# Performance work log

Hardware: AMD Instinct MI355X
Metric: run time of the kernel (lower is better)

## Reference

```python
import jax, jax.numpy as jnp
import numpy as np

N = 384      # max_nodes
H = 256      # layers[0] == layers[1] == layers[2]
Z = 128      # dim_z
ED = 128     # edge_dim
AH = ED // 2 # attention hidden

# complete directed graph: combinations (i<j) then reversed pairs
_i, _j = np.triu_indices(N, k=1)
_SRC = jnp.asarray(np.concatenate([_i, _j]), dtype=jnp.int32)  # edge_index[0]
_DST = jnp.asarray(np.concatenate([_j, _i]), dtype=jnp.int32)  # edge_index[1]


def setup_inputs() -> dict:
    key = jax.random.key(0)
    ks = jax.random.split(key, 16)
    def p(k, shape, fan_in):
        return jax.random.normal(k, shape, dtype=jnp.float32) * (1.0 / np.sqrt(fan_in))
    return {
        "z": jax.random.normal(ks[0], (1, Z), dtype=jnp.float32),
        # GRU (torch layout: W_ih [3H, Z], W_hh [3H, H]; gate order r, z, n)
        "gru_Wih": p(ks[1], (3 * H, Z), Z),
        "gru_Whh": p(ks[2], (3 * H, H), H),
        "gru_bih": jnp.zeros((3 * H,), jnp.float32),
        "gru_bhh": jnp.zeros((3 * H,), jnp.float32),
        # edge_generator MLP: 2H -> 4H -> ED
        "eg_W1": p(ks[3], (2 * H, 4 * H), 2 * H), "eg_b1": jnp.zeros((4 * H,), jnp.float32),
        "eg_W2": p(ks[4], (4 * H, ED), 4 * H),   "eg_b2": jnp.zeros((ED,), jnp.float32),
        # attention MLPs: (ED+H) -> ED//2 -> 1
        "att0_W1": p(ks[5], (ED + H, AH), ED + H), "att0_b1": jnp.zeros((AH,), jnp.float32),
        "att0_W2": p(ks[6], (AH, 1), AH),           "att0_b2": jnp.zeros((1,), jnp.float32),
        "att1_W1": p(ks[7], (ED + H, AH), ED + H), "att1_b1": jnp.zeros((AH,), jnp.float32),
        "att1_W2": p(ks[8], (AH, 1), AH),           "att1_b2": jnp.zeros((1,), jnp.float32),
        # EdgeConv output linears: H -> H
        "conv0_W": p(ks[9], (H, H), H),  "conv0_b": jnp.zeros((H,), jnp.float32),
        "conv1_W": p(ks[10], (H, H), H), "conv1_b": jnp.zeros((H,), jnp.float32),
    }


def _forward(z, gru_Wih, gru_Whh, gru_bih, gru_bhh,
             eg_W1, eg_b1, eg_W2, eg_b2,
             att0_W1, att0_b1, att0_W2, att0_b2,
             att1_W1, att1_b1, att1_W2, att1_b2,
             conv0_W, conv0_b, conv1_W, conv1_b):
    # --- GRU node generation: input is the same latent z at every step ---
    gi = z[0] @ gru_Wih.T + gru_bih            # [3H], constant per step
    gir, giz, gin = jnp.split(gi, 3)
    def step(h, _):
        gh = h @ gru_Whh.T + gru_bhh
        ghr, ghz, ghn = jnp.split(gh, 3)
        r = jax.nn.sigmoid(gir + ghr)
        u = jax.nn.sigmoid(giz + ghz)
        n = jnp.tanh(gin + r * ghn)
        h2 = (1.0 - u) * n + u * h
        return h2, h2
    _, nodes = jax.lax.scan(step, jnp.zeros((H,), z.dtype), None, length=N)  # [N, H]

    # --- edge features over the complete directed graph ---
    pairs = jnp.concatenate([nodes[_SRC], nodes[_DST]], axis=-1)            # [E, 2H]
    edges = jax.nn.relu(pairs @ eg_W1 + eg_b1) @ eg_W2 + eg_b2              # [E, ED]

    # --- EdgeConv: gather src, attention MLP gate, scatter-sum, linear ---
    def conv(x, aW1, ab1, aW2, ab2, W, b):
        xs = x[_SRC]                                                        # [E, H]
        a_in = jnp.concatenate([edges, xs], axis=-1)                        # [E, ED+H]
        att = jax.nn.sigmoid(jax.nn.relu(a_in @ aW1 + ab1) @ aW2 + ab2)     # [E, 1]
        agg = jax.ops.segment_sum(att * xs, _DST, num_segments=N)           # [N, H]
        return agg @ W + b

    x = jax.nn.relu(conv(nodes, att0_W1, att0_b1, att0_W2, att0_b2, conv0_W, conv0_b))
    x = conv(x, att1_W1, att1_b1, att1_W2, att1_b2, conv1_W, conv1_b)
    return jnp.sum(x, axis=0)                                               # [H]


def reference(z, gru_Wih, gru_Whh, gru_bih, gru_bhh,
              eg_W1, eg_b1, eg_W2, eg_b2,
              att0_W1, att0_b1, att0_W2, att0_b2,
              att1_W1, att1_b1, att1_W2, att1_b2,
              conv0_W, conv0_b, conv1_W, conv1_b):
    return _forward(z, gru_Wih, gru_Whh, gru_bih, gru_bhh,
                    eg_W1, eg_b1, eg_W2, eg_b2,
                    att0_W1, att0_b1, att0_W2, att0_b2,
                    att1_W1, att1_b1, att1_W2, att1_b2,
                    conv0_W, conv0_b, conv1_W, conv1_b)
```

## Files before the change

### kernel.cpp

```cpp
#include <hip/hip_runtime.h>
#include <hip/hip_fp16.h>
#include <cstdint>

#define DEV static __device__ __forceinline__

typedef _Float16 h2v __attribute__((ext_vector_type(2)));
typedef _Float16 half8 __attribute__((ext_vector_type(8)));
typedef float float4v __attribute__((ext_vector_type(4)));

union U32H2 { uint32_t u; _Float16 f[2]; };

DEV uint32_t pack_f2(float a, float b) {
    auto p = __builtin_amdgcn_cvt_pkrtz(a, b);
    return __builtin_bit_cast(uint32_t, p);
}

DEV half8 bc8(uint4 v) { return __builtin_bit_cast(half8, v); }

DEV float sigmoidf_(float x) { return 1.0f / (1.0f + __expf(-x)); }

DEV void gl_lds16(const void* gsrc, void* ldst) {
    __builtin_amdgcn_global_load_lds(
        (const __attribute__((address_space(1))) uint32_t*)gsrc,
        (__attribute__((address_space(3))) uint32_t*)ldst, 16, 0, 0);
}

DEV float pick4(float4v lo, float4v hi, int bsel, int r) {
    float v0 = bsel ? hi[0] : lo[0];
    float v1 = bsel ? hi[1] : lo[1];
    float v2 = bsel ? hi[2] : lo[2];
    float v3 = bsel ? hi[3] : lo[3];
    float x01 = (r & 1) ? v1 : v0;
    float x23 = (r & 1) ? v3 : v2;
    return (r & 2) ? x23 : x01;
}

static const size_t OFF_W16T  = 0;
static const size_t OFF_GI    = 98304;
static const size_t OFF_CC    = 99072;
static const size_t OFF_BF    = 99200;
static const size_t OFF_NODES = 164736;
static const size_t OFF_PF    = 263040;
static const size_t OFF_QF    = 459648;
static const size_t OFF_R0    = 656256;
static const size_t OFF_R1    = 680832;
static const size_t OFF_TT    = 705408;
static const size_t OFF_ATT0  = 10142592;
static const size_t OFF_ATT1  = 10290048;
static const size_t OFF_AGG   = 10437504;
static const size_t OFF_X0    = 10535808;
static const size_t OFF_CS    = 10634112;
static const size_t OFF_V     = 10634496;
static const size_t WS_TOTAL  = 10634752;

__global__ void k_prep_all(const float* __restrict__ Whh, uint32_t* __restrict__ WL,
                           const float* __restrict__ z, const float* __restrict__ Wih,
                           const float* __restrict__ bih, const float* __restrict__ bhh,
                           float* __restrict__ gs,
                           const float* __restrict__ egb2, const float* __restrict__ a0W1,
                           const float* __restrict__ a1W1, float* __restrict__ cc,
                           const float* __restrict__ egW2, uint32_t* __restrict__ BF) {
    int bb = blockIdx.x;
    if (bb < 96) {
        int o4 = bb * 256 + threadIdx.x;
        int c = o4 >> 9, t = o4 & 511;
        int rt = c >> 3, kt = c & 7;
        int lane = t & 63, wv = t >> 6;
        int row = (rt >> 1) * 256 + wv * 32 + ((rt & 1) << 4) + (lane & 15);
        int k0 = kt*32 + (lane >> 4)*8;
        const float* src = Whh + row*256 + k0;
        uint4 o;
        o.x = pack_f2(src[0], src[1]);
        o.y = pack_f2(src[2], src[3]);
        o.z = pack_f2(src[4], src[5]);
        o.w = pack_f2(src[6], src[7]);
        ((uint4*)WL)[o4] = o;
    } else if (bb < 99) {
        int o = (bb - 96) * 256 + threadIdx.x;
        float acc = bih[o];
        if (o < 512) acc += bhh[o];
        for (int i = 0; i < 128; ++i) acc += Wih[o*128 + i] * z[i];
        gs[o] = acc;
    } else if (bb == 99) {
        int t = threadIdx.x;
        if (t < 128) {
            const float* A = (t < 64) ? a0W1 : a1W1;
            int j = t & 63;
            float acc = 0.f;
            for (int i = 0; i < 128; ++i) acc += egb2[i] * A[i*64 + j];
            cc[t] = acc;
        }
    } else {
        int idx = (bb - 100) * 256 + threadIdx.x;
        int k2 = idx >> 7, n = idx & 127;
        const float* A = (n < 64) ? (a0W1 + n) : (a1W1 + (n - 64));
        const float* w0 = egW2 + (2*k2) * 128;
        float a = 0.f, b = 0.f;
        for (int i = 0; i < 128; ++i) {
            float av = A[i*64];
            a += w0[i] * av;
            b += w0[128 + i] * av;
        }
        int kk = k2 >> 4, jgrp = (k2 >> 2) & 3, sub = k2 & 3;
        int lane = jgrp*16 + (n & 15), t = n >> 4;
        BF[((kk*8 + t)*64 + lane)*4 + sub] = pack_f2(a, b);
    }
}

__global__ void __launch_bounds__(512, 2)
k_gru(const float* __restrict__ gs, const float* __restrict__ bhh,
      const uint32_t* __restrict__ WL, float* __restrict__ nodes) {
    int tid = threadIdx.x;
    int lane = tid & 63, wv = tid >> 6;
    int kq = lane >> 4, c = lane & 15;
    __shared__ __align__(16) _Float16 hh16[512];

    uint4 w[48];
    const uint4* wl4 = (const uint4*)WL;
    #pragma unroll
    for (int cc = 0; cc < 48; ++cc) w[cc] = wl4[cc*512 + tid];
    #pragma unroll
    for (int cc = 0; cc < 48; ++cc)
        asm volatile("" : "+a"(w[cc].x), "+a"(w[cc].y), "+a"(w[cc].z), "+a"(w[cc].w));

    const float L2E = 1.44269504088896f;
    int r = c & 3, bsel = (c >> 2) & 1;
    int i_loc = kq*4 + r + bsel*16;
    int gidx = wv*32 + i_loc;
    float pr = -L2E * gs[gidx];
    float pz = -L2E * gs[256 + gidx];
    float gin_l = gs[512 + gidx];
    float bn_l  = bhh[512 + gidx];
    float pn = -2.f * L2E * gin_l;
    bool active = (c < 8);

    float h = 0.f;
    if (tid < 256) ((uint32_t*)hh16)[tid] = 0u;
    __syncthreads();

    const float4v z4 = {0.f, 0.f, 0.f, 0.f};
    int par = 0;
    for (int t = 0; t < 384; ++t) {
        const _Float16* hb = hh16 + par*256 + kq*8;
        uint4 b[8];
        #pragma unroll
        for (int kt = 0; kt < 8; ++kt) b[kt] = *(const uint4*)(hb + kt*32);

        float4v d0, d1, d2, d3, d4, d5;
        d0 = __builtin_amdgcn_mfma_f32_16x16x32_f16(bc8(w[0]),  bc8(b[0]), z4, 0, 0, 0);
        d1 = __builtin_amdgcn_mfma_f32_16x16x32_f16(bc8(w[8]),  bc8(b[0]), z4, 0, 0, 0);
        #pragma unroll
        for (int kt = 1; kt < 8; ++kt) {
            d0 = __builtin_amdgcn_mfma_f32_16x16x32_f16(bc8(w[kt]),    bc8(b[kt]), d0, 0, 0, 0);
            d1 = __builtin_amdgcn_mfma_f32_16x16x32_f16(bc8(w[8+kt]),  bc8(b[kt]), d1, 0, 0, 0);
        }
        float ghr = pick4(d0, d1, bsel, r);
        float er = __builtin_amdgcn_exp2f(__builtin_fmaf(ghr, -L2E, pr));
        float rg = __builtin_amdgcn_rcpf(1.f + er);

        d2 = __builtin_amdgcn_mfma_f32_16x16x32_f16(bc8(w[16]), bc8(b[0]), z4, 0, 0, 0);
        d3 = __builtin_amdgcn_mfma_f32_16x16x32_f16(bc8(w[24]), bc8(b[0]), z4, 0, 0, 0);
        d4 = __builtin_amdgcn_mfma_f32_16x16x32_f16(bc8(w[32]), bc8(b[0]), z4, 0, 0, 0);
        d5 = __builtin_amdgcn_mfma_f32_16x16x32_f16(bc8(w[40]), bc8(b[0]), z4, 0, 0, 0);
        #pragma unroll
        for (int kt = 1; kt < 8; ++kt) {
            d2 = __builtin_amdgcn_mfma_f32_16x16x32_f16(bc8(w[16+kt]), bc8(b[kt]), d2, 0, 0, 0);
            d3 = __builtin_amdgcn_mfma_f32_16x16x32_f16(bc8(w[24+kt]), bc8(b[kt]), d3, 0, 0, 0);
            d4 = __builtin_amdgcn_mfma_f32_16x16x32_f16(bc8(w[32+kt]), bc8(b[kt]), d4, 0, 0, 0);
            d5 = __builtin_amdgcn_mfma_f32_16x16x32_f16(bc8(w[40+kt]), bc8(b[kt]), d5, 0, 0, 0);
        }

        float ghz = pick4(d2, d3, bsel, r);
        float ghn = pick4(d4, d5, bsel, r);
        float eu = __builtin_amdgcn_exp2f(__builtin_fmaf(ghz, -L2E, pz));
        float u  = __builtin_amdgcn_rcpf(1.f + eu);
        float tm = ghn + bn_l;
        float q  = __builtin_fmaf(rg * tm, -2.f * L2E, pn);
        float e2 = __builtin_amdgcn_exp2f(q);
        float nn = __builtin_fmaf(2.f, __builtin_amdgcn_rcpf(1.f + e2), -1.f);
        h = nn + u * (h - nn);

        if (active) {
            hh16[(par ^ 1)*256 + gidx] = (_Float16)h;
            nodes[t*256 + gidx] = h;
        }
        asm volatile("s_waitcnt lgkmcnt(0)" ::: "memory");
        __builtin_amdgcn_sched_barrier(0);
        __builtin_amdgcn_s_barrier();
        __builtin_amdgcn_sched_barrier(0);
        par ^= 1;
    }
}

__global__ void k_pq(const float* __restrict__ nodes, const float* __restrict__ eg_W1,
                     const float* __restrict__ eg_b1, const float* __restrict__ a0W1,
                     const float* __restrict__ a0b1, const float* __restrict__ cc,
                     uint32_t* __restrict__ PF, uint32_t* __restrict__ QF,
                     float* __restrict__ R0) {
    int tid = threadIdx.x;
    int s0 = blockIdx.x * 4;
    __shared__ float ns[4][256];
    #pragma unroll
    for (int q = 0; q < 4; ++q) ns[q][tid] = nodes[(s0+q)*256 + tid];
    __syncthreads();

    int k0 = tid * 4;
    float acc[4][4];
    #pragma unroll
    for (int q = 0; q < 4; ++q) { acc[q][0]=0;acc[q][1]=0;acc[q][2]=0;acc[q][3]=0; }
    for (int i = 0; i < 256; ++i) {
        float4 wv = *(const float4*)&eg_W1[i*1024 + k0];
        #pragma unroll
        for (int q = 0; q < 4; ++q) {
            float nv = ns[q][i];
            acc[q][0] += nv*wv.x; acc[q][1] += nv*wv.y;
            acc[q][2] += nv*wv.z; acc[q][3] += nv*wv.w;
        }
    }
    float4 bv = *(const float4*)&eg_b1[k0];
    {
        int kk = k0 >> 5;
        int lgrp = ((k0 >> 3) & 3) * 16;
        int sub = (k0 & 7) >> 1;
        #pragma unroll
        for (int q = 0; q < 4; ++q) {
            int s = s0 + q, g = s >> 4, srow = s & 15;
            uint2 pw;
            pw.x = pack_f2(acc[q][0] + bv.x, acc[q][1] + bv.y);
            pw.y = pack_f2(acc[q][2] + bv.z, acc[q][3] + bv.w);
            *(uint2*)(PF + (((g*32 + kk)*64 + lgrp + srow) << 2) + sub) = pw;
        }
    }

    #pragma unroll
    for (int q = 0; q < 4; ++q) { acc[q][0]=0;acc[q][1]=0;acc[q][2]=0;acc[q][3]=0; }
    for (int i = 0; i < 256; ++i) {
        float4 wv = *(const float4*)&eg_W1[(256+i)*1024 + k0];
        #pragma unroll
        for (int q = 0; q < 4; ++q) {
            float nv = ns[q][i];
            acc[q][0] += nv*wv.x; acc[q][1] += nv*wv.y;
            acc[q][2] += nv*wv.z; acc[q][3] += nv*wv.w;
        }
    }
    #pragma unroll
    for (int q = 0; q < 4; ++q) {
        uint2 pw;
        pw.x = pack_f2(acc[q][0], acc[q][1]);
        pw.y = pack_f2(acc[q][2], acc[q][3]);
        ((uint2*)QF)[(s0+q)*256 + tid] = pw;
    }

    int srow = tid >> 6, j = tid & 63;
    float racc = a0b1[j] + cc[j];
    for (int i = 0; i < 256; ++i) racc += ns[srow][i] * a0W1[(128+i)*64 + j];
    R0[(s0+srow)*64 + j] = racc;
}

DEV void stageA(const uint32_t* __restrict__ PF, const uint32_t* __restrict__ BF,
                int g, int hc, char* buf, int tid) {
    const char* psrc = (const char*)(PF + ((size_t)g*32 + (size_t)hc*2) * 256);
    if (tid < 128) gl_lds16(psrc + tid*16, buf + tid*16);
    const char* bsrc = (const char*)(BF + (size_t)hc * 4096);
    #pragma unroll
    for (int i = 0; i < 4; ++i)
        gl_lds16(bsrc + tid*16 + i*4096, buf + 2048 + tid*16 + i*4096);
}

__global__ void __launch_bounds__(256, 2)
k_phaseA_mfma(const uint32_t* __restrict__ PF, const uint32_t* __restrict__ QF,
              const uint32_t* __restrict__ BF, uint32_t* __restrict__ TT) {
    __shared__ __align__(16) char smem[69632];
    uint4* Qs4 = (uint4*)smem;
    char* bufbase = smem + 32768;

    int tid = threadIdx.x;
    int lane = tid & 63, wv = tid >> 6;
    int g = blockIdx.x, d0 = blockIdx.y * 16;

    {
        const char* src = (const char*)(QF + (size_t)d0 * 512);
        int off = tid * 16;
        #pragma unroll
        for (int i = 0; i < 8; ++i)
            gl_lds16(src + off + i*4096, (char*)Qs4 + off + i*4096);
    }
    stageA(PF, BF, g, 0, bufbase, tid);
    asm volatile("s_waitcnt vmcnt(0)" ::: "memory");
    __builtin_amdgcn_sched_barrier(0);
    __builtin_amdgcn_s_barrier();
    __builtin_amdgcn_sched_barrier(0);

    float4v acc[4][8];
    #pragma unroll
    for (int t = 0; t < 4; ++t)
        #pragma unroll
        for (int n = 0; n < 8; ++n) acc[t][n] = 0.f;

    for (int hc = 0; hc < 16; ++hc) {
        char* cur = bufbase + (hc & 1) * 18432;
        char* nxt = bufbase + ((hc + 1) & 1) * 18432;
        if (hc < 15) stageA(PF, BF, g, hc + 1, nxt, tid);

        uint4* Ph = (uint4*)cur;
        uint4* Bh = (uint4*)(cur + 2048);
        #pragma unroll
        for (int kkl = 0; kkl < 2; ++kkl) {
            int kkg = hc*2 + kkl;
            half8 b[8];
            #pragma unroll
            for (int n = 0; n < 8; ++n) b[n] = bc8(Bh[(kkl*8 + n)*64 + lane]);
            half8 p8 = bc8(Ph[kkl*64 + lane]);
            #pragma unroll
            for (int t = 0; t < 4; ++t) {
                half8 q8 = bc8(Qs4[(wv*4 + t)*128 + kkg*4 + (lane >> 4)]);
                half8 x = p8 + q8;
                half8 zz = 0;
                x = __builtin_elementwise_max(x, zz);
                #pragma unroll
                for (int n = 0; n < 8; ++n)
                    acc[t][n] = __builtin_amdgcn_mfma_f32_16x16x32_f16(x, b[n], acc[t][n], 0, 0, 0);
            }
        }
        asm volatile("s_waitcnt vmcnt(0)" ::: "memory");
        __builtin_amdgcn_sched_barrier(0);
        __builtin_amdgcn_s_barrier();
        __builtin_amdgcn_sched_barrier(0);
    }

    _Float16* epi = (_Float16*)(smem + 32768);
    int cn = lane & 15, rhi = (lane >> 4) * 4;
    for (int half = 0; half < 2; ++half) {
        __syncthreads();
        #pragma unroll
        for (int t = 0; t < 4; ++t) {
            int dl = wv*4 + t;
            #pragma unroll
            for (int n = 0; n < 4; ++n) {
                int j = n*16 + cn;
                float4v v = acc[t][half*4 + n];
                #pragma unroll
                for (int r = 0; r < 4; ++r)
                    epi[((rhi + r)*16 + dl)*64 + j] = (_Float16)v[r];
            }
        }
        __syncthreads();
        int srow = tid >> 4, dl = tid & 15;
        const uint4* src = (const uint4*)(epi + tid*64);
        uint4* dst = (uint4*)(TT + ((size_t)((g*16 + srow)*384 + d0 + dl))*64 + half*32);
        #pragma unroll
        for (int q = 0; q < 8; ++q) dst[q] = src[q];
    }
}

__global__ void k_att(const uint32_t* __restrict__ TT, const float* __restrict__ R,
                      const float* __restrict__ w2, const float* __restrict__ b2,
                      int off, float* __restrict__ ATT, float* __restrict__ CS) {
    int tid = threadIdx.x;
    int p = blockIdx.x * 256 + tid;
    int s = p / 384, d = p - s * 384;
    int sa = (blockIdx.x * 256) / 384;
    __shared__ float w2s[64];
    __shared__ float rs[2][64];
    if (tid < 64) w2s[tid] = w2[tid];
    else if (tid < 128) rs[0][tid - 64] = R[sa*64 + (tid - 64)];
    else if (tid < 192) {
        int sb = sa + 1;
        rs[1][tid - 128] = (sb < 384) ? R[sb*64 + (tid - 128)] : 0.f;
    }
    __syncthreads();
    const uint4* tp = (const uint4*)(TT + (size_t)p*64 + off);
    const float* rp = (s == sa) ? rs[0] : rs[1];
    float logit = b2[0];
    #pragma unroll
    for (int m = 0; m < 8; ++m) {
        uint4 tv = tp[m];
        uint32_t us[4] = {tv.x, tv.y, tv.z, tv.w};
        #pragma unroll
        for (int q = 0; q < 4; ++q) {
            U32H2 c; c.u = us[q];
            int j = m*8 + q*2;
            float h0 = fmaxf((float)c.f[0] + rp[j],   0.f);
            float h1 = fmaxf((float)c.f[1] + rp[j+1], 0.f);
            logit += h0*w2s[j] + h1*w2s[j+1];
        }
    }
    float a = 1.f / (1.f + __expf(-logit));
    float a_eff = (s == d) ? 0.f : a;
    ATT[p] = a_eff;

    if (CS) {
        float va = (s == sa) ? a_eff : 0.f;
        float vb = (s != sa) ? a_eff : 0.f;
        #pragma unroll
        for (int o = 32; o > 0; o >>= 1) {
            va += __shfl_down(va, o, 64);
            vb += __shfl_down(vb, o, 64);
        }
        if ((tid & 63) == 0) {
            atomicAdd(&CS[sa], va);
            int sb = sa + 1;
            if (sb < 384) atomicAdd(&CS[sb], vb);
        }
    }
}

__global__ void __launch_bounds__(256)
k_agg(const float* __restrict__ ATT, const float* __restrict__ X,
      float* __restrict__ AGG) {
    int tid = threadIdx.x;
    int d0 = blockIdx.x * 16;
    __shared__ float att_s[16][17];
    float acc[16];
    #pragma unroll
    for (int dl = 0; dl < 16; ++dl) acc[dl] = 0.f;

    for (int s0 = 0; s0 < 384; s0 += 16) {
        __syncthreads();
        {
            int row = tid >> 4, col = tid & 15;
            att_s[row][col] = ATT[(s0 + row)*384 + d0 + col];
        }
        __syncthreads();
        #pragma unroll 4
        for (int ss = 0; ss < 16; ++ss) {
            float x = X[(s0 + ss)*256 + tid];
            #pragma unroll
            for (int dl = 0; dl < 16; ++dl) acc[dl] += att_s[ss][dl] * x;
        }
    }
    #pragma unroll
    for (int dl = 0; dl < 16; ++dl)
        AGG[(d0 + dl)*256 + tid] = acc[dl];
}

__global__ void k_x0r1(const float* __restrict__ AGG, const float* __restrict__ W,
                       const float* __restrict__ b, const float* __restrict__ a1W1,
                       const float* __restrict__ a1b1, const float* __restrict__ cc,
                       float* __restrict__ X0, float* __restrict__ R1) {
    int d = blockIdx.x, tid = threadIdx.x;
    __shared__ float ag[256];
    __shared__ float xs[256];
    ag[tid] = AGG[d*256 + tid];
    __syncthreads();
    float acc = b[tid];
    for (int i = 0; i < 256; ++i) acc += ag[i] * W[i*256 + tid];
    acc = fmaxf(acc, 0.f);
    X0[d*256 + tid] = acc;
    xs[tid] = acc;
    __syncthreads();
    if (tid < 64) {
        float r = a1b1[tid] + cc[64 + tid];
        for (int i = 0; i < 256; ++i) r += xs[i] * a1W1[(128+i)*64 + tid];
        R1[d*64 + tid] = r;
    }
}

__global__ void k_vout(const float* __restrict__ CS, const float* __restrict__ X0,
                       const float* __restrict__ W, const float* __restrict__ b,
                       float* __restrict__ out) {
    int tid = threadIdx.x;
    __shared__ float cs[384];
    __shared__ float vs[256];
    for (int q = tid; q < 384; q += 256) cs[q] = CS[q];
    __syncthreads();
    float acc = 0.f;
    for (int s = 0; s < 384; s += 4) {
        acc += cs[s]*X0[s*256 + tid] + cs[s+1]*X0[(s+1)*256 + tid]
             + cs[s+2]*X0[(s+2)*256 + tid] + cs[s+3]*X0[(s+3)*256 + tid];
    }
    vs[tid] = acc;
    __syncthreads();
    float o = 384.f * b[tid];
    for (int i = 0; i < 256; ++i) o += vs[i] * W[i*256 + tid];
    out[tid] = o;
}

extern "C" void kernel_launch(void* const* d_in, const int* in_sizes, int n_in,
                              void* d_out, int out_size, void* d_ws, size_t ws_size,
                              hipStream_t stream) {
    if (ws_size < WS_TOTAL * sizeof(uint32_t)) return;

    const float* z    = (const float*)d_in[0];
    const float* Wih  = (const float*)d_in[1];
    const float* Whh  = (const float*)d_in[2];
    const float* bih  = (const float*)d_in[3];
    const float* bhh  = (const float*)d_in[4];
    const float* egW1 = (const float*)d_in[5];
    const float* egb1 = (const float*)d_in[6];
    const float* egW2 = (const float*)d_in[7];
    const float* egb2 = (const float*)d_in[8];
    const float* a0W1 = (const float*)d_in[9];
    const float* a0b1 = (const float*)d_in[10];
    const float* a0W2 = (const float*)d_in[11];
    const float* a0b2 = (const float*)d_in[12];
    const float* a1W1 = (const float*)d_in[13];
    const float* a1b1 = (const float*)d_in[14];
    const float* a1W2 = (const float*)d_in[15];
    const float* a1b2 = (const float*)d_in[16];
    const float* c0W  = (const float*)d_in[17];
    const float* c0b  = (const float*)d_in[18];
    const float* c1W  = (const float*)d_in[19];
    const float* c1b  = (const float*)d_in[20];

    uint32_t* ws   = (uint32_t*)d_ws;
    uint32_t* WL   = ws + OFF_W16T;
    float*    gi   = (float*)(ws + OFF_GI);
    float*    cc   = (float*)(ws + OFF_CC);
    uint32_t* BF   = ws + OFF_BF;
    float*    nodes= (float*)(ws + OFF_NODES);
    uint32_t* PF   = ws + OFF_PF;
    uint32_t* QF   = ws + OFF_QF;
    float*    R0   = (float*)(ws + OFF_R0);
    float*    R1   = (float*)(ws + OFF_R1);
    uint32_t* TT   = ws + OFF_TT;
    float*    ATT0 = (float*)(ws + OFF_ATT0);
    float*    ATT1 = (float*)(ws + OFF_ATT1);
    float*    AGG  = (float*)(ws + OFF_AGG);
    float*    X0   = (float*)(ws + OFF_X0);
    float*    CS   = (float*)(ws + OFF_CS);
    float*    out  = (float*)d_out;

    hipMemsetAsync(CS, 0, 384 * sizeof(float), stream);
    hipLaunchKernelGGL(k_prep_all,    dim3(356), dim3(256), 0, stream,
                       Whh, WL, z, Wih, bih, bhh, gi, egb2, a0W1, a1W1, cc, egW2, BF);
    hipLaunchKernelGGL(k_gru,         dim3(1),   dim3(512), 0, stream, gi, bhh, WL, nodes);
    hipLaunchKernelGGL(k_pq,          dim3(96),  dim3(256), 0, stream, nodes, egW1, egb1, a0W1, a0b1, cc, PF, QF, R0);
    hipLaunchKernelGGL(k_phaseA_mfma, dim3(24, 24), dim3(256), 0, stream, PF, QF, BF, TT);
    hipLaunchKernelGGL(k_att,         dim3(576), dim3(256), 0, stream, TT, R0, a0W2, a0b2, 0,  ATT0, (float*)nullptr);
    hipLaunchKernelGGL(k_agg,         dim3(24),  dim3(256), 0, stream, ATT0, nodes, AGG);
    hipLaunchKernelGGL(k_x0r1,        dim3(384), dim3(256), 0, stream, AGG, c0W, c0b, a1W1, a1b1, cc, X0, R1);
    hipLaunchKernelGGL(k_att,         dim3(576), dim3(256), 0, stream, TT, R1, a1W2, a1b2, 32, ATT1, CS);
    hipLaunchKernelGGL(k_vout,        dim3(1),   dim3(256), 0, stream, CS, X0, c1W, c1b, out);
}
```

Before: 699.5 us.

## Fuse attention-0 into phaseA epilogue, merge agg with x0, overlap BF prep with GRU

Reorganizes the pipeline. BF/cc preparation now runs in extra blocks of the GRU launch so it overlaps the serial single-block GRU. The first attention sigmoid is computed in the phaseA epilogue directly from the fp16 tile in LDS, which removes a separate pass over TT. phaseA moves to 512 threads with fewer rows per wave, and the aggregation is merged into the x0/R1 kernel per destination node. This cuts kernel launches and global traffic, at the cost of more epilogue work, different occupancy, and a per-node aggregation that rereads X for every node.

```diff
diff --git a/kernel.cpp b/kernel.cpp
--- a/kernel.cpp
+++ b/kernel.cpp
@@ -16,8 +16,6 @@
 }
 
 DEV half8 bc8(uint4 v) { return __builtin_bit_cast(half8, v); }
-
-DEV float sigmoidf_(float x) { return 1.0f / (1.0f + __expf(-x)); }
 
 DEV void gl_lds16(const void* gsrc, void* ldst) {
     __builtin_amdgcn_global_load_lds(
@@ -50,22 +48,17 @@
 static const size_t OFF_AGG   = 10437504;
 static const size_t OFF_X0    = 10535808;
 static const size_t OFF_CS    = 10634112;
-static const size_t OFF_V     = 10634496;
-static const size_t WS_TOTAL  = 10634752;
-
-__global__ void k_prep_all(const float* __restrict__ Whh, uint32_t* __restrict__ WL,
-                           const float* __restrict__ z, const float* __restrict__ Wih,
-                           const float* __restrict__ bih, const float* __restrict__ bhh,
-                           float* __restrict__ gs,
-                           const float* __restrict__ egb2, const float* __restrict__ a0W1,
-                           const float* __restrict__ a1W1, float* __restrict__ cc,
-                           const float* __restrict__ egW2, uint32_t* __restrict__ BF) {
-    int bb = blockIdx.x;
-    if (bb < 96) {
-        int o4 = bb * 256 + threadIdx.x;
-        int c = o4 >> 9, t = o4 & 511;
+static const size_t WS_TOTAL  = 10634816;
+
+__global__ void k_prep_wl(const float* __restrict__ Whh, uint32_t* __restrict__ WL,
+                          const float* __restrict__ z, const float* __restrict__ Wih,
+                          const float* __restrict__ bih, const float* __restrict__ bhh,
+                          float* __restrict__ gs) {
+    int bb = blockIdx.x, tid = threadIdx.x;
+    if (bb < 48) {
+        int c = bb;
         int rt = c >> 3, kt = c & 7;
-        int lane = t & 63, wv = t >> 6;
+        int lane = tid & 63, wv = tid >> 6;
         int row = (rt >> 1) * 256 + wv * 32 + ((rt & 1) << 4) + (lane & 15);
         int k0 = kt*32 + (lane >> 4)*8;
         const float* src = Whh + row*256 + k0;
@@ -74,24 +67,105 @@
         o.y = pack_f2(src[2], src[3]);
         o.z = pack_f2(src[4], src[5]);
         o.w = pack_f2(src[6], src[7]);
-        ((uint4*)WL)[o4] = o;
-    } else if (bb < 99) {
-        int o = (bb - 96) * 256 + threadIdx.x;
-        float acc = bih[o];
-        if (o < 512) acc += bhh[o];
-        for (int i = 0; i < 128; ++i) acc += Wih[o*128 + i] * z[i];
-        gs[o] = acc;
-    } else if (bb == 99) {
-        int t = threadIdx.x;
-        if (t < 128) {
-            const float* A = (t < 64) ? a0W1 : a1W1;
-            int j = t & 63;
-            float acc = 0.f;
-            for (int i = 0; i < 128; ++i) acc += egb2[i] * A[i*64 + j];
-            cc[t] = acc;
-        }
+        ((uint4*)WL)[c*512 + tid] = o;
     } else {
-        int idx = (bb - 100) * 256 + threadIdx.x;
+        int o = (bb - 48) * 512 + tid;
+        if (o < 768) {
+            float acc = bih[o];
+            if (o < 512) acc += bhh[o];
+            for (int i = 0; i < 128; ++i) acc += Wih[o*128 + i] * z[i];
+            gs[o] = acc;
+        }
+    }
+}
+
+__global__ void __launch_bounds__(512, 2)
+k_gru_bf(const float* __restrict__ gs, const float* __restrict__ bhh,
+         const uint32_t* __restrict__ WL, float* __restrict__ nodes,
+         const float* __restrict__ egW2, const float* __restrict__ egb2,
+         const float* __restrict__ a0W1, const float* __restrict__ a1W1,
+         uint32_t* __restrict__ BF, float* __restrict__ cc) {
+    int bb = blockIdx.x, tid = threadIdx.x;
+    if (bb == 0) {
+        __shared__ __align__(16) _Float16 hh16[512];
+        int lane = tid & 63, wv = tid >> 6;
+        int kq = lane >> 4, c = lane & 15;
+        const float L2E = 1.44269504088896f;
+        int r = c & 3, bsel = (c >> 2) & 1;
+        int gidx = wv*32 + kq*4 + r + bsel*16;
+        bool active = (c < 8);
+
+        uint4 w[48];
+        const uint4* wl4 = (const uint4*)WL;
+        #pragma unroll
+        for (int q = 0; q < 48; ++q) w[q] = wl4[q*512 + tid];
+        #pragma unroll
+        for (int q = 0; q < 48; ++q)
+            asm volatile("" : "+a"(w[q].x), "+a"(w[q].y), "+a"(w[q].z), "+a"(w[q].w));
+
+        float pr = -L2E * gs[gidx];
+        float pz = -L2E * gs[256 + gidx];
+        float pn = -2.f * L2E * gs[512 + gidx];
+        float bn_l = bhh[512 + gidx];
+
+        float h = 0.f;
+        if (tid < 256) ((uint32_t*)hh16)[tid] = 0u;
+        __syncthreads();
+
+        const float4v z4 = {0.f, 0.f, 0.f, 0.f};
+        int par = 0;
+        for (int t = 0; t < 384; ++t) {
+            const _Float16* hb = hh16 + par*256 + kq*8;
+            uint4 b[8];
+            #pragma unroll
+            for (int kt = 0; kt < 8; ++kt) b[kt] = *(const uint4*)(hb + kt*32);
+
+            float4v d0, d1, d2, d3, d4, d5;
+            d0 = __builtin_amdgcn_mfma_f32_16x16x32_f16(bc8(w[0]),  bc8(b[0]), z4, 0, 0, 0);
+            d1 = __builtin_amdgcn_mfma_f32_16x16x32_f16(bc8(w[8]),  bc8(b[0]), z4, 0, 0, 0);
+            #pragma unroll
+            for (int kt = 1; kt < 8; ++kt) {
+                d0 = __builtin_amdgcn_mfma_f32_16x16x32_f16(bc8(w[kt]),   bc8(b[kt]), d0, 0, 0, 0);
+                d1 = __builtin_amdgcn_mfma_f32_16x16x32_f16(bc8(w[8+kt]), bc8(b[kt]), d1, 0, 0, 0);
+            }
+            float ghr = pick4(d0, d1, bsel, r);
+            float er = __builtin_amdgcn_exp2f(__builtin_fmaf(ghr, -L2E, pr));
+            float rg = __builtin_amdgcn_rcpf(1.f + er);
+
+            d2 = __builtin_amdgcn_mfma_f32_16x16x32_f16(bc8(w[16]), bc8(b[0]), z4, 0, 0, 0);
+            d3 = __builtin_amdgcn_mfma_f32_16x16x32_f16(bc8(w[24]), bc8(b[0]), z4, 0, 0, 0);
+            d4 = __builtin_amdgcn_mfma_f32_16x16x32_f16(bc8(w[32]), bc8(b[0]), z4, 0, 0, 0);
+            d5 = __builtin_amdgcn_mfma_f32_16x16x32_f16(bc8(w[40]), bc8(b[0]), z4, 0, 0, 0);
+            #pragma unroll
+            for (int kt = 1; kt < 8; ++kt) {
+                d2 = __builtin_amdgcn_mfma_f32_16x16x32_f16(bc8(w[16+kt]), bc8(b[kt]), d2, 0, 0, 0);
+                d3 = __builtin_amdgcn_mfma_f32_16x16x32_f16(bc8(w[24+kt]), bc8(b[kt]), d3, 0, 0, 0);
+                d4 = __builtin_amdgcn_mfma_f32_16x16x32_f16(bc8(w[32+kt]), bc8(b[kt]), d4, 0, 0, 0);
+                d5 = __builtin_amdgcn_mfma_f32_16x16x32_f16(bc8(w[40+kt]), bc8(b[kt]), d5, 0, 0, 0);
+            }
+
+            float ghz = pick4(d2, d3, bsel, r);
+            float ghn = pick4(d4, d5, bsel, r);
+            float eu = __builtin_amdgcn_exp2f(__builtin_fmaf(ghz, -L2E, pz));
+            float u  = __builtin_amdgcn_rcpf(1.f + eu);
+            float tm = ghn + bn_l;
+            float q  = __builtin_fmaf(rg * tm, -2.f * L2E, pn);
+            float e2 = __builtin_amdgcn_exp2f(q);
+            float nn = __builtin_fmaf(2.f, __builtin_amdgcn_rcpf(1.f + e2), -1.f);
+            h = nn + u * (h - nn);
+
+            if (active) {
+                hh16[(par ^ 1)*256 + gidx] = (_Float16)h;
+                nodes[t*256 + gidx] = h;
+            }
+            asm volatile("s_waitcnt lgkmcnt(0)" ::: "memory");
+            __builtin_amdgcn_sched_barrier(0);
+            __builtin_amdgcn_s_barrier();
+            __builtin_amdgcn_sched_barrier(0);
+            par ^= 1;
+        }
+    } else if (bb < 129) {
+        int idx = (bb - 1) * 512 + tid;
         int k2 = idx >> 7, n = idx & 127;
         const float* A = (n < 64) ? (a0W1 + n) : (a1W1 + (n - 64));
         const float* w0 = egW2 + (2*k2) * 128;
@@ -104,91 +178,14 @@
         int kk = k2 >> 4, jgrp = (k2 >> 2) & 3, sub = k2 & 3;
         int lane = jgrp*16 + (n & 15), t = n >> 4;
         BF[((kk*8 + t)*64 + lane)*4 + sub] = pack_f2(a, b);
-    }
-}
-
-__global__ void __launch_bounds__(512, 2)
-k_gru(const float* __restrict__ gs, const float* __restrict__ bhh,
-      const uint32_t* __restrict__ WL, float* __restrict__ nodes) {
-    int tid = threadIdx.x;
-    int lane = tid & 63, wv = tid >> 6;
-    int kq = lane >> 4, c = lane & 15;
-    __shared__ __align__(16) _Float16 hh16[512];
-
-    uint4 w[48];
-    const uint4* wl4 = (const uint4*)WL;
-    #pragma unroll
-    for (int cc = 0; cc < 48; ++cc) w[cc] = wl4[cc*512 + tid];
-    #pragma unroll
-    for (int cc = 0; cc < 48; ++cc)
-        asm volatile("" : "+a"(w[cc].x), "+a"(w[cc].y), "+a"(w[cc].z), "+a"(w[cc].w));
-
-    const float L2E = 1.44269504088896f;
-    int r = c & 3, bsel = (c >> 2) & 1;
-    int i_loc = kq*4 + r + bsel*16;
-    int gidx = wv*32 + i_loc;
-    float pr = -L2E * gs[gidx];
-    float pz = -L2E * gs[256 + gidx];
-    float gin_l = gs[512 + gidx];
-    float bn_l  = bhh[512 + gidx];
-    float pn = -2.f * L2E * gin_l;
-    bool active = (c < 8);
-
-    float h = 0.f;
-    if (tid < 256) ((uint32_t*)hh16)[tid] = 0u;
-    __syncthreads();
-
-    const float4v z4 = {0.f, 0.f, 0.f, 0.f};
-    int par = 0;
-    for (int t = 0; t < 384; ++t) {
-        const _Float16* hb = hh16 + par*256 + kq*8;
-        uint4 b[8];
-        #pragma unroll
-        for (int kt = 0; kt < 8; ++kt) b[kt] = *(const uint4*)(hb + kt*32);
-
-        float4v d0, d1, d2, d3, d4, d5;
-        d0 = __builtin_amdgcn_mfma_f32_16x16x32_f16(bc8(w[0]),  bc8(b[0]), z4, 0, 0, 0);
-        d1 = __builtin_amdgcn_mfma_f32_16x16x32_f16(bc8(w[8]),  bc8(b[0]), z4, 0, 0, 0);
-        #pragma unroll
-        for (int kt = 1; kt < 8; ++kt) {
-            d0 = __builtin_amdgcn_mfma_f32_16x16x32_f16(bc8(w[kt]),    bc8(b[kt]), d0, 0, 0, 0);
-            d1 = __builtin_amdgcn_mfma_f32_16x16x32_f16(bc8(w[8+kt]),  bc8(b[kt]), d1, 0, 0, 0);
-        }
-        float ghr = pick4(d0, d1, bsel, r);
-        float er = __builtin_amdgcn_exp2f(__builtin_fmaf(ghr, -L2E, pr));
-        float rg = __builtin_amdgcn_rcpf(1.f + er);
-
-        d2 = __builtin_amdgcn_mfma_f32_16x16x32_f16(bc8(w[16]), bc8(b[0]), z4, 0, 0, 0);
-        d3 = __builtin_amdgcn_mfma_f32_16x16x32_f16(bc8(w[24]), bc8(b[0]), z4, 0, 0, 0);
-        d4 = __builtin_amdgcn_mfma_f32_16x16x32_f16(bc8(w[32]), bc8(b[0]), z4, 0, 0, 0);
-        d5 = __builtin_amdgcn_mfma_f32_16x16x32_f16(bc8(w[40]), bc8(b[0]), z4, 0, 0, 0);
-        #pragma unroll
-        for (int kt = 1; kt < 8; ++kt) {
-            d2 = __builtin_amdgcn_mfma_f32_16x16x32_f16(bc8(w[16+kt]), bc8(b[kt]), d2, 0, 0, 0);
-            d3 = __builtin_amdgcn_mfma_f32_16x16x32_f16(bc8(w[24+kt]), bc8(b[kt]), d3, 0, 0, 0);
-            d4 = __builtin_amdgcn_mfma_f32_16x16x32_f16(bc8(w[32+kt]), bc8(b[kt]), d4, 0, 0, 0);
-            d5 = __builtin_amdgcn_mfma_f32_16x16x32_f16(bc8(w[40+kt]), bc8(b[kt]), d5, 0, 0, 0);
-        }
-
-        float ghz = pick4(d2, d3, bsel, r);
-        float ghn = pick4(d4, d5, bsel, r);
-        float eu = __builtin_amdgcn_exp2f(__builtin_fmaf(ghz, -L2E, pz));
-        float u  = __builtin_amdgcn_rcpf(1.f + eu);
-        float tm = ghn + bn_l;
-        float q  = __builtin_fmaf(rg * tm, -2.f * L2E, pn);
-        float e2 = __builtin_amdgcn_exp2f(q);
-        float nn = __builtin_fmaf(2.f, __builtin_amdgcn_rcpf(1.f + e2), -1.f);
-        h = nn + u * (h - nn);
-
-        if (active) {
-            hh16[(par ^ 1)*256 + gidx] = (_Float16)h;
-            nodes[t*256 + gidx] = h;
-        }
-        asm volatile("s_waitcnt lgkmcnt(0)" ::: "memory");
-        __builtin_amdgcn_sched_barrier(0);
-        __builtin_amdgcn_s_barrier();
-        __builtin_amdgcn_sched_barrier(0);
-        par ^= 1;
+    } else {
+        if (tid < 128) {
+            const float* A = (tid < 64) ? a0W1 : a1W1;
+            int j = tid & 63;
+            float acc = 0.f;
+            for (int i = 0; i < 128; ++i) acc += egb2[i] * A[i*64 + j];
+            cc[tid] = acc;
+        }
     }
 }
 
@@ -257,51 +254,53 @@
     R0[(s0+srow)*64 + j] = racc;
 }
 
-DEV void stageA(const uint32_t* __restrict__ PF, const uint32_t* __restrict__ BF,
-                int g, int hc, char* buf, int tid) {
-    const char* psrc = (const char*)(PF + ((size_t)g*32 + (size_t)hc*2) * 256);
-    if (tid < 128) gl_lds16(psrc + tid*16, buf + tid*16);
-    const char* bsrc = (const char*)(BF + (size_t)hc * 4096);
-    #pragma unroll
-    for (int i = 0; i < 4; ++i)
-        gl_lds16(bsrc + tid*16 + i*4096, buf + 2048 + tid*16 + i*4096);
-}
-
-__global__ void __launch_bounds__(256, 2)
-k_phaseA_mfma(const uint32_t* __restrict__ PF, const uint32_t* __restrict__ QF,
-              const uint32_t* __restrict__ BF, uint32_t* __restrict__ TT) {
+__global__ void __launch_bounds__(512, 4)
+k_phaseA(const uint32_t* __restrict__ PF, const uint32_t* __restrict__ QF,
+         const uint32_t* __restrict__ BF, const float* __restrict__ R0,
+         const float* __restrict__ a0W2, const float* __restrict__ a0b2,
+         uint32_t* __restrict__ TT, float* __restrict__ ATT0) {
     __shared__ __align__(16) char smem[69632];
     uint4* Qs4 = (uint4*)smem;
     char* bufbase = smem + 32768;
-
     int tid = threadIdx.x;
     int lane = tid & 63, wv = tid >> 6;
-    int g = blockIdx.x, d0 = blockIdx.y * 16;
+    int g = blockIdx.x, dt = blockIdx.y, d0 = dt * 16;
 
     {
         const char* src = (const char*)(QF + (size_t)d0 * 512);
-        int off = tid * 16;
-        #pragma unroll
-        for (int i = 0; i < 8; ++i)
-            gl_lds16(src + off + i*4096, (char*)Qs4 + off + i*4096);
-    }
-    stageA(PF, BF, g, 0, bufbase, tid);
+        for (int off = tid*16; off < 32768; off += 8192)
+            gl_lds16(src + off, (char*)Qs4 + off);
+    }
+    {
+        const char* psrc = (const char*)(PF + (size_t)g * 8192);
+        if (tid < 128) gl_lds16(psrc + tid*16, bufbase + tid*16);
+        const char* bsrc = (const char*)BF;
+        #pragma unroll
+        for (int i = 0; i < 2; ++i)
+            gl_lds16(bsrc + tid*16 + i*8192, bufbase + 2048 + tid*16 + i*8192);
+    }
     asm volatile("s_waitcnt vmcnt(0)" ::: "memory");
     __builtin_amdgcn_sched_barrier(0);
     __builtin_amdgcn_s_barrier();
     __builtin_amdgcn_sched_barrier(0);
 
-    float4v acc[4][8];
+    float4v acc[2][8];
     #pragma unroll
-    for (int t = 0; t < 4; ++t)
+    for (int t = 0; t < 2; ++t)
         #pragma unroll
         for (int n = 0; n < 8; ++n) acc[t][n] = 0.f;
 
     for (int hc = 0; hc < 16; ++hc) {
         char* cur = bufbase + (hc & 1) * 18432;
         char* nxt = bufbase + ((hc + 1) & 1) * 18432;
-        if (hc < 15) stageA(PF, BF, g, hc + 1, nxt, tid);
-
+        if (hc < 15) {
+            const char* psrc = (const char*)(PF + ((size_t)g*32 + (size_t)(hc+1)*2) * 256);
+            if (tid < 128) gl_lds16(psrc + tid*16, nxt + tid*16);
+            const char* bsrc = (const char*)(BF + (size_t)(hc+1) * 4096);
+            #pragma unroll
+            for (int i = 0; i < 2; ++i)
+                gl_lds16(bsrc + tid*16 + i*8192, nxt + 2048 + tid*16 + i*8192);
+        }
         uint4* Ph = (uint4*)cur;
         uint4* Bh = (uint4*)(cur + 2048);
         #pragma unroll
@@ -312,8 +311,8 @@
             for (int n = 0; n < 8; ++n) b[n] = bc8(Bh[(kkl*8 + n)*64 + lane]);
             half8 p8 = bc8(Ph[kkl*64 + lane]);
             #pragma unroll
-            for (int t = 0; t < 4; ++t) {
-                half8 q8 = bc8(Qs4[(wv*4 + t)*128 + kkg*4 + (lane >> 4)]);
+            for (int t = 0; t < 2; ++t) {
+                half8 q8 = bc8(Qs4[(wv*2 + t)*128 + kkg*4 + (lane >> 4)]);
                 half8 x = p8 + q8;
                 half8 zz = 0;
                 x = __builtin_elementwise_max(x, zz);
@@ -328,13 +327,21 @@
         __builtin_amdgcn_sched_barrier(0);
     }
 
+    __syncthreads();
+    float* R0s = (float*)smem;
+    float* w2s = (float*)(smem + 4096);
+    for (int i = tid; i < 1024; i += 512)
+        R0s[i] = R0[(size_t)(g*16 + (i >> 6))*64 + (i & 63)];
+    if (tid < 64) w2s[tid] = a0W2[tid];
+    float b2v = a0b2[0];
+
     _Float16* epi = (_Float16*)(smem + 32768);
     int cn = lane & 15, rhi = (lane >> 4) * 4;
     for (int half = 0; half < 2; ++half) {
         __syncthreads();
         #pragma unroll
-        for (int t = 0; t < 4; ++t) {
-            int dl = wv*4 + t;
+        for (int t = 0; t < 2; ++t) {
+            int dl = wv*2 + t;
             #pragma unroll
             for (int n = 0; n < 4; ++n) {
                 int j = n*16 + cn;
@@ -345,11 +352,26 @@
             }
         }
         __syncthreads();
-        int srow = tid >> 4, dl = tid & 15;
-        const uint4* src = (const uint4*)(epi + tid*64);
-        uint4* dst = (uint4*)(TT + ((size_t)((g*16 + srow)*384 + d0 + dl))*64 + half*32);
-        #pragma unroll
-        for (int q = 0; q < 8; ++q) dst[q] = src[q];
+        {
+            int p = tid >> 1, sub = tid & 1;
+            int srow = p >> 4, dl = p & 15;
+            const uint4* src = (const uint4*)(epi + (size_t)p*64);
+            uint4* dst = (uint4*)(TT + ((size_t)((g*16 + srow)*384 + d0 + dl))*64 + half*32);
+            #pragma unroll
+            for (int q = 0; q < 4; ++q) dst[sub*4 + q] = src[sub*4 + q];
+        }
+        if (half == 0 && tid < 256) {
+            int sl = tid >> 4, dl = tid & 15;
+            const _Float16* tp = epi + (size_t)(sl*16 + dl)*64;
+            const float* rp = R0s + sl*64;
+            float logit = b2v;
+            #pragma unroll
+            for (int j = 0; j < 64; ++j)
+                logit += fmaxf((float)tp[j] + rp[j], 0.f) * w2s[j];
+            float a = 1.f / (1.f + __expf(-logit));
+            int s = g*16 + sl, d = d0 + dl;
+            ATT0[(size_t)s*384 + d] = (s == d) ? 0.f : a;
+        }
     }
 }
 
@@ -406,53 +428,33 @@
 }
 
 __global__ void __launch_bounds__(256)
-k_agg(const float* __restrict__ ATT, const float* __restrict__ X,
-      float* __restrict__ AGG) {
-    int tid = threadIdx.x;
-    int d0 = blockIdx.x * 16;
-    __shared__ float att_s[16][17];
-    float acc[16];
-    #pragma unroll
-    for (int dl = 0; dl < 16; ++dl) acc[dl] = 0.f;
-
-    for (int s0 = 0; s0 < 384; s0 += 16) {
-        __syncthreads();
-        {
-            int row = tid >> 4, col = tid & 15;
-            att_s[row][col] = ATT[(s0 + row)*384 + d0 + col];
-        }
-        __syncthreads();
-        #pragma unroll 4
-        for (int ss = 0; ss < 16; ++ss) {
-            float x = X[(s0 + ss)*256 + tid];
-            #pragma unroll
-            for (int dl = 0; dl < 16; ++dl) acc[dl] += att_s[ss][dl] * x;
-        }
-    }
-    #pragma unroll
-    for (int dl = 0; dl < 16; ++dl)
-        AGG[(d0 + dl)*256 + tid] = acc[dl];
-}
-
-__global__ void k_x0r1(const float* __restrict__ AGG, const float* __restrict__ W,
-                       const float* __restrict__ b, const float* __restrict__ a1W1,
-                       const float* __restrict__ a1b1, const float* __restrict__ cc,
-                       float* __restrict__ X0, float* __restrict__ R1) {
+k_aggx0(const float* __restrict__ ATT, const float* __restrict__ X,
+        const float* __restrict__ W, const float* __restrict__ b,
+        const float* __restrict__ a1W1, const float* __restrict__ a1b1,
+        const float* __restrict__ cc,
+        float* __restrict__ X0, float* __restrict__ R1) {
     int d = blockIdx.x, tid = threadIdx.x;
+    __shared__ float att_col[384];
     __shared__ float ag[256];
     __shared__ float xs[256];
-    ag[tid] = AGG[d*256 + tid];
-    __syncthreads();
-    float acc = b[tid];
-    for (int i = 0; i < 256; ++i) acc += ag[i] * W[i*256 + tid];
-    acc = fmaxf(acc, 0.f);
-    X0[d*256 + tid] = acc;
-    xs[tid] = acc;
+    for (int s = tid; s < 384; s += 256) att_col[s] = ATT[(size_t)s*384 + d];
+    __syncthreads();
+    float acc = 0.f;
+    #pragma unroll 4
+    for (int s = 0; s < 384; ++s)
+        acc += att_col[s] * X[(size_t)s*256 + tid];
+    ag[tid] = acc;
+    __syncthreads();
+    float x0 = b[tid];
+    for (int i = 0; i < 256; ++i) x0 += ag[i] * W[i*256 + tid];
+    x0 = fmaxf(x0, 0.f);
+    X0[(size_t)d*256 + tid] = x0;
+    xs[tid] = x0;
     __syncthreads();
     if (tid < 64) {
         float r = a1b1[tid] + cc[64 + tid];
         for (int i = 0; i < 256; ++i) r += xs[i] * a1W1[(128+i)*64 + tid];
-        R1[d*64 + tid] = r;
+        R1[(size_t)d*64 + tid] = r;
     }
 }
 
@@ -505,7 +507,7 @@
 
     uint32_t* ws   = (uint32_t*)d_ws;
     uint32_t* WL   = ws + OFF_W16T;
-    float*    gi   = (float*)(ws + OFF_GI);
+    float*    gs   = (float*)(ws + OFF_GI);
     float*    cc   = (float*)(ws + OFF_CC);
     uint32_t* BF   = ws + OFF_BF;
     float*    nodes= (float*)(ws + OFF_NODES);
@@ -516,20 +518,17 @@
     uint32_t* TT   = ws + OFF_TT;
     float*    ATT0 = (float*)(ws + OFF_ATT0);
     float*    ATT1 = (float*)(ws + OFF_ATT1);
-    float*    AGG  = (float*)(ws + OFF_AGG);
     float*    X0   = (float*)(ws + OFF_X0);
     float*    CS   = (float*)(ws + OFF_CS);
     float*    out  = (float*)d_out;
 
     hipMemsetAsync(CS, 0, 384 * sizeof(float), stream);
-    hipLaunchKernelGGL(k_prep_all,    dim3(356), dim3(256), 0, stream,
-                       Whh, WL, z, Wih, bih, bhh, gi, egb2, a0W1, a1W1, cc, egW2, BF);
-    hipLaunchKernelGGL(k_gru,         dim3(1),   dim3(512), 0, stream, gi, bhh, WL, nodes);
-    hipLaunchKernelGGL(k_pq,          dim3(96),  dim3(256), 0, stream, nodes, egW1, egb1, a0W1, a0b1, cc, PF, QF, R0);
-    hipLaunchKernelGGL(k_phaseA_mfma, dim3(24, 24), dim3(256), 0, stream, PF, QF, BF, TT);
-    hipLaunchKernelGGL(k_att,         dim3(576), dim3(256), 0, stream, TT, R0, a0W2, a0b2, 0,  ATT0, (float*)nullptr);
-    hipLaunchKernelGGL(k_agg,         dim3(24),  dim3(256), 0, stream, ATT0, nodes, AGG);
-    hipLaunchKernelGGL(k_x0r1,        dim3(384), dim3(256), 0, stream, AGG, c0W, c0b, a1W1, a1b1, cc, X0, R1);
-    hipLaunchKernelGGL(k_att,         dim3(576), dim3(256), 0, stream, TT, R1, a1W2, a1b2, 32, ATT1, CS);
-    hipLaunchKernelGGL(k_vout,        dim3(1),   dim3(256), 0, stream, CS, X0, c1W, c1b, out);
-}
+    hipLaunchKernelGGL(k_prep_wl, dim3(50),     dim3(512), 0, stream, Whh, WL, z, Wih, bih, bhh, gs);
+    hipLaunchKernelGGL(k_gru_bf,  dim3(130),    dim3(512), 0, stream, gs, bhh, WL, nodes,
+                       egW2, egb2, a0W1, a1W1, BF, cc);
+    hipLaunchKernelGGL(k_pq,      dim3(96),     dim3(256), 0, stream, nodes, egW1, egb1, a0W1, a0b1, cc, PF, QF, R0);
+    hipLaunchKernelGGL(k_phaseA,  dim3(24, 24), dim3(512), 0, stream, PF, QF, BF, R0, a0W2, a0b2, TT, ATT0);
+    hipLaunchKernelGGL(k_aggx0,   dim3(384),    dim3(256), 0, stream, ATT0, nodes, c0W, c0b, a1W1, a1b1, cc, X0, R1);
+    hipLaunchKernelGGL(k_att,     dim3(576),    dim3(256), 0, stream, TT, R1, a1W2, a1b2, 32, ATT1, CS);
+    hipLaunchKernelGGL(k_vout,    dim3(1),      dim3(256), 0, stream, CS, X0, c1W, c1b, out);
+}
```

Result: faster. 668.9 us (-4.4%).
